# Kernel optimization log

Measured on AMD Instinct MI355X. Metric: run time of the kernel, lower is better.

Reference implementation:

```python
import jax, jax.numpy as jnp
import numpy as np

D_MODEL = 2048
D_INNER = 4096
D_XB = 512
D_STATE = 16
D_CONV = 4
DT_RANK = 128
BATCH = 1
SEQ = 2048
NUM_XB_HEAD = D_XB // D_STATE      # 32 kv heads
NUM_C_HEAD = D_INNER // D_STATE    # 256 query-side heads (groups)
REPEAT = NUM_C_HEAD // NUM_XB_HEAD # 8
HEAD_P = D_INNER // NUM_C_HEAD     # channels per group (= d_state here)


def setup_inputs() -> dict:
    key = jax.random.key(0)
    ks = jax.random.split(key, 8)
    sc = lambda k, shape, s=0.02: (jax.random.normal(k, shape, jnp.float32) * s)
    hidden_states = jax.random.normal(ks[0], (BATCH, SEQ, D_MODEL), jnp.float32)
    in_proj_w = sc(ks[1], (2 * D_XB + 2 * D_INNER, D_MODEL))
    dt_in_proj_w = sc(ks[2], (DT_RANK, D_MODEL))
    dt_proj_w = sc(ks[3], (D_INNER, DT_RANK), DT_RANK ** -0.5)
    # standard mamba dt bias init: inv-softplus of dt ~ logUniform[1e-3, 0.1]
    dt = jnp.exp(jax.random.uniform(ks[4], (D_INNER,)) * (np.log(0.1) - np.log(1e-3)) + np.log(1e-3))
    dt_proj_b = dt + jnp.log(-jnp.expm1(-dt))
    conv_w = sc(ks[5], (D_INNER, 1, D_CONV), 0.2)
    conv_b = jnp.zeros((D_INNER,), jnp.float32)
    A_log = jnp.log(jnp.tile(jnp.arange(1, D_STATE + 1, dtype=jnp.float32), (D_INNER, 1)))
    D = jnp.ones((D_INNER,), jnp.float32)
    out_proj_w = sc(ks[6], (D_MODEL, D_INNER), D_INNER ** -0.5)
    return dict(hidden_states=hidden_states, in_proj_w=in_proj_w, dt_in_proj_w=dt_in_proj_w,
                dt_proj_w=dt_proj_w, dt_proj_b=dt_proj_b, conv_w=conv_w, conv_b=conv_b,
                A_log=A_log, D=D, out_proj_w=out_proj_w)


def _mamba2_fwd(hidden_states, in_proj_w, dt_in_proj_w, dt_proj_w, dt_proj_b,
                conv_w, conv_b, A_log, D, out_proj_w):
    b, l, _ = hidden_states.shape
    zxbc = hidden_states @ in_proj_w.T  # (b,l,2*d_xb+2*d_inner)
    z = zxbc[..., :D_INNER]
    x = zxbc[..., D_INNER:D_INNER + D_XB]
    Bm = zxbc[..., D_INNER + D_XB:D_INNER + 2 * D_XB]
    Cm = zxbc[..., D_INNER + 2 * D_XB:]
    A = -jnp.exp(A_log)  # (d_inner, d_state)
    # low-rank dt: d_model -> dt_rank -> d_inner
    dt = (hidden_states @ dt_in_proj_w.T) @ dt_proj_w.T  # (b,l,d_inner)
    delta = jax.nn.softplus(dt + dt_proj_b)  # delta_softplus with delta_bias
    # repeat_kv before conv: (b,l,h_xb,n) -> (b,l,h_C,n) -> (b,d_inner,l)
    xh = jnp.repeat(x.reshape(b, l, NUM_XB_HEAD, D_STATE), REPEAT, axis=2)
    xc = xh.reshape(b, l, D_INNER).transpose(0, 2, 1)  # (b,d,l)
    # depthwise causal conv1d + SiLU
    xc = jax.lax.conv_general_dilated(xc, conv_w, (1,), [(D_CONV - 1, 0)],
                                      feature_group_count=D_INNER,
                                      dimension_numbers=('NCH', 'OIH', 'NCH'))
    u = jax.nn.silu(xc + conv_b[None, :, None])  # (b,d,l)
    Bh = jnp.repeat(Bm.reshape(b, l, NUM_XB_HEAD, D_STATE), REPEAT, axis=2)  # (b,l,g,n)
    Ch = Cm.reshape(b, l, NUM_C_HEAD, D_STATE)  # (b,l,g,n)
    # selective scan over time; channel d -> group d // HEAD_P
    u_r = u.transpose(0, 2, 1).reshape(b, l, NUM_C_HEAD, HEAD_P)
    d_r = delta.reshape(b, l, NUM_C_HEAD, HEAD_P)
    A_r = A.reshape(NUM_C_HEAD, HEAD_P, D_STATE)

    def step(h, inp):
        dt_t, u_t, B_t, C_t = inp  # (b,g,p),(b,g,p),(b,g,n),(b,g,n)
        dA = jnp.exp(dt_t[..., None] * A_r)  # (b,g,p,n)
        h = h * dA + (dt_t * u_t)[..., None] * B_t[:, :, None, :]
        y = jnp.einsum('bgpn,bgn->bgp', h, C_t)
        return h, y

    h0 = jnp.zeros((b, NUM_C_HEAD, HEAD_P, D_STATE), u.dtype)
    xs = (d_r.transpose(1, 0, 2, 3), u_r.transpose(1, 0, 2, 3),
          Bh.transpose(1, 0, 2, 3), Ch.transpose(1, 0, 2, 3))
    _, ys = jax.lax.scan(step, h0, xs)  # (l,b,g,p)
    y = ys.transpose(1, 0, 2, 3).reshape(b, l, D_INNER)
    y = y + u.transpose(0, 2, 1) * D  # skip D*u
    out = y * jax.nn.silu(z)          # gate
    return out @ out_proj_w.T         # (b,l,d_model)


def reference(hidden_states, in_proj_w, dt_in_proj_w, dt_proj_w, dt_proj_b,
              conv_w, conv_b, A_log, D, out_proj_w):
    return _mamba2_fwd(hidden_states, in_proj_w, dt_in_proj_w, dt_proj_w, dt_proj_b,
                       conv_w, conv_b, A_log, D, out_proj_w)
```

## Files before the change

kernel.cpp:

```cpp
#include <hip/hip_runtime.h>
#include <hip/hip_bf16.h>

#define SEQ     2048
#define DMODEL  2048
#define DINNER  4096
#define DXB     512
#define DSTATE  16
#define DTRANK  128
#define ZXBC_N  9216
#define NGROUP  256
#define NCH     32
#define TC      64

#define OFF_Z 0
#define OFF_X 4096
#define OFF_B 4608
#define OFF_C 5120

typedef __attribute__((ext_vector_type(8))) short short8;
typedef __attribute__((ext_vector_type(8))) unsigned short us8;
typedef __attribute__((ext_vector_type(4))) float f32x4;

__device__ __forceinline__ float softplus_f(float x) {
    return x > 0.f ? x + log1pf(expf(-x)) : log1pf(expf(x));
}
__device__ __forceinline__ float silu_f(float x) {
    return x / (1.f + __expf(-x));
}
__device__ __forceinline__ ushort f2bf(float f) {
    union { float f; unsigned u; } v; v.f = f;
    unsigned r = v.u + 0x7fffu + ((v.u >> 16) & 1u);
    return (ushort)(r >> 16);
}
__device__ __forceinline__ float bf2f(ushort u) {
    union { unsigned u; float f; } v; v.u = (unsigned)u << 16;
    return v.f;
}

__global__ __launch_bounds__(256) void f32_to_bf16(const float* __restrict__ in,
                                                   ushort* __restrict__ out, int n4) {
    int i = blockIdx.x * 256 + threadIdx.x;
    if (i < n4) {
        float4 v = ((const float4*)in)[i];
        ushort4 o;
        o.x = f2bf(v.x); o.y = f2bf(v.y); o.z = f2bf(v.z); o.w = f2bf(v.w);
        ((ushort4*)out)[i] = o;
    }
}

__global__ __launch_bounds__(256) void cvt4_kernel(const float* __restrict__ h,   ushort* __restrict__ hb,
                                                   const float* __restrict__ ip,  ushort* __restrict__ ipb,
                                                   const float* __restrict__ di,  ushort* __restrict__ dib,
                                                   const float* __restrict__ dp,  ushort* __restrict__ dpb) {
    const int b = blockIdx.x;
    const float* src; ushort* dst; int off;
    if (b < 4096)        { src = h;  dst = hb;  off = b; }
    else if (b < 22528)  { src = ip; dst = ipb; off = b - 4096; }
    else if (b < 22784)  { src = di; dst = dib; off = b - 22528; }
    else                 { src = dp; dst = dpb; off = b - 22784; }
    const int i = off * 256 + threadIdx.x;
    float4 v = ((const float4*)src)[i];
    ushort4 o;
    o.x = f2bf(v.x); o.y = f2bf(v.y); o.z = f2bf(v.z); o.w = f2bf(v.w);
    ((ushort4*)dst)[i] = o;
}

#define GLOAD16(gp, lp) __builtin_amdgcn_global_load_lds( \
    (const __attribute__((address_space(1))) void*)(gp), \
    (__attribute__((address_space(3))) void*)(lp), 16, 0, 0)

template<int EPI>
__global__ __launch_bounds__(256, 4) void gemm_bt_bf16(const ushort* __restrict__ A,
                                                       const ushort* __restrict__ B,
                                                       void* __restrict__ Cout,
                                                       const float* __restrict__ bias,
                                                       int M, int N, int K) {
    __shared__ ushort As[128 * 64];
    __shared__ ushort Bs[128 * 64];
    const int nbx = N >> 7;
    const int nwg = gridDim.x;
    int lin = blockIdx.x;
    if ((nwg & 7) == 0) lin = (lin & 7) * (nwg >> 3) + (lin >> 3);
    const int by = lin / nbx;
    const int bx = lin - by * nbx;
    const int row0 = by << 7, col0 = bx << 7;

    const int tid  = threadIdx.x;
    const int w    = tid >> 6;
    const int lane = tid & 63;
    const size_t kstride = (size_t)K * gridDim.y;
    const size_t koff    = (size_t)blockIdx.y * K;
    const size_t cbase   = (size_t)blockIdx.y * M * N;

    const int lrow  = lane >> 3;
    const int lslot = (lane & 7) ^ lrow;
    const ushort* ag = A + (size_t)(row0 + (w << 5) + lrow) * kstride + koff + (lslot << 3);
    const ushort* bg = B + (size_t)(col0 + (w << 5) + lrow) * kstride + koff + (lslot << 3);
    ushort* asb = As + ((w << 5) << 6);
    ushort* bsb = Bs + ((w << 5) << 6);

    const int wm = (w >> 1) << 6;
    const int wn = (w & 1) << 6;
    const int fr = lane & 15;
    const int kq = lane >> 4;
    const int f7 = fr & 7;

    f32x4 acc[4][4] = {};
    for (int k0 = 0; k0 < K; k0 += 64) {
        __syncthreads();
        #pragma unroll
        for (int k = 0; k < 4; ++k) {
            GLOAD16(ag + (size_t)(k << 3) * kstride + k0, asb + (k << 9));
            GLOAD16(bg + (size_t)(k << 3) * kstride + k0, bsb + (k << 9));
        }
        __syncthreads();
        #pragma unroll
        for (int ks = 0; ks < 2; ++ks) {
            const int ps = (((ks << 2) + kq) ^ f7) << 3;
            short8 af[4], bf[4];
            #pragma unroll
            for (int i = 0; i < 4; ++i)
                af[i] = *(const short8*)(As + ((wm + i * 16 + fr) << 6) + ps);
            #pragma unroll
            for (int j = 0; j < 4; ++j)
                bf[j] = *(const short8*)(Bs + ((wn + j * 16 + fr) << 6) + ps);
            #pragma unroll
            for (int i = 0; i < 4; ++i)
                #pragma unroll
                for (int j = 0; j < 4; ++j)
                    acc[i][j] = __builtin_amdgcn_mfma_f32_16x16x32_bf16(af[i], bf[j], acc[i][j], 0, 0, 0);
        }
    }

    const int orow = row0 + wm + (kq << 2);
    const int ocol = col0 + wn + fr;
    #pragma unroll
    for (int i = 0; i < 4; ++i) {
        #pragma unroll
        for (int r = 0; r < 4; ++r) {
            const int row = orow + i * 16 + r;
            #pragma unroll
            for (int j = 0; j < 4; ++j) {
                const int col = ocol + j * 16;
                float v = acc[i][j][r];
                if (EPI == 1) v = softplus_f(v + bias[col]);
                if (EPI == 2) ((ushort*)Cout)[(size_t)row * N + col] = f2bf(v);
                else          ((float*)Cout)[cbase + (size_t)row * N + col] = v;
            }
        }
    }
}

__global__ __launch_bounds__(256) void t1_reduce(const float* __restrict__ part,
                                                 ushort* __restrict__ out) {
    const int i = blockIdx.x * 256 + threadIdx.x;
    float4 s = ((const float4*)part)[i];
    #pragma unroll
    for (int z = 1; z < 8; ++z) {
        float4 p = ((const float4*)part)[z * 65536 + i];
        s.x += p.x; s.y += p.y; s.z += p.z; s.w += p.w;
    }
    ushort4 o;
    o.x = f2bf(s.x); o.y = f2bf(s.y); o.z = f2bf(s.z); o.w = f2bf(s.w);
    ((ushort4*)out)[i] = o;
}

__global__ __launch_bounds__(256) void out_reduce2(const float* __restrict__ part,
                                                   float* __restrict__ out) {
    const int i = blockIdx.x * 256 + threadIdx.x;
    float4 a = ((const float4*)part)[i];
    float4 b = ((const float4*)part)[1048576 + i];
    a.x += b.x; a.y += b.y; a.z += b.z; a.w += b.w;
    ((float4*)out)[i] = a;
}


__global__ __launch_bounds__(256) void scan_pass1(const ushort* __restrict__ zxbc,
                                                  const float* __restrict__ delta,
                                                  const float* __restrict__ conv_w,
                                                  const float* __restrict__ conv_b,
                                                  const float* __restrict__ A_log,
                                                  float* __restrict__ hend,
                                                  float* __restrict__ dsum) {
    __shared__ float sB[TC][32];
    const int ch  = blockIdx.y;
    const int c0  = blockIdx.x << 8;
    const int tid = threadIdx.x;
    const int c   = c0 + tid;
    const int t0  = ch * TC;
    const int xhl = (tid >> 7) & 1;
    const int xcol = ((c >> 7) << 4) | (c & 15);

    float Av[16];
    #pragma unroll
    for (int q = 0; q < 4; ++q) {
        float4 a4 = *(const float4*)(A_log + (c << 4) + (q << 2));
        Av[q*4+0] = -expf(a4.x); Av[q*4+1] = -expf(a4.y);
        Av[q*4+2] = -expf(a4.z); Av[q*4+3] = -expf(a4.w);
    }
    const float4 w4 = *(const float4*)(conv_w + c * 4);
    const float cb = conv_b[c];

    {
        const int f  = tid & 3;
        const int tl = tid >> 2;
        const int xb0 = (c0 >> 7) << 4;
        us8 v = *(const us8*)(zxbc + (size_t)(t0 + tl) * ZXBC_N + OFF_B + xb0 + (f << 3));
        float* dst = &sB[tl][f << 3];
        #pragma unroll
        for (int e = 0; e < 8; ++e) dst[e] = bf2f(v[e]);
    }

    float xm3 = 0.f, xm2 = 0.f, xm1 = 0.f;
    if (ch > 0) {
        xm3 = bf2f(zxbc[(size_t)(t0 - 3) * ZXBC_N + OFF_X + xcol]);
        xm2 = bf2f(zxbc[(size_t)(t0 - 2) * ZXBC_N + OFF_X + xcol]);
        xm1 = bf2f(zxbc[(size_t)(t0 - 1) * ZXBC_N + OFF_X + xcol]);
    }
    float dcur = delta[(size_t)t0 * DINNER + c];
    float xcur = bf2f(zxbc[(size_t)t0 * ZXBC_N + OFF_X + xcol]);

    float h[16];
    #pragma unroll
    for (int n = 0; n < 16; ++n) h[n] = 0.f;
    float Dc = 0.f;
    __syncthreads();

    #pragma unroll 4
    for (int tl = 0; tl < TC; ++tl) {
        float dn = 0.f, xn = 0.f;
        if (tl < TC - 1) {
            const size_t t1 = (size_t)(t0 + tl + 1);
            dn = delta[t1 * DINNER + c];
            xn = bf2f(zxbc[t1 * ZXBC_N + OFF_X + xcol]);
        }
        float Bv[16];
        *(float4*)(Bv +  0) = *(const float4*)&sB[tl][(xhl << 4) +  0];
        *(float4*)(Bv +  4) = *(const float4*)&sB[tl][(xhl << 4) +  4];
        *(float4*)(Bv +  8) = *(const float4*)&sB[tl][(xhl << 4) +  8];
        *(float4*)(Bv + 12) = *(const float4*)&sB[tl][(xhl << 4) + 12];
        float u = cb;
        u = fmaf(w4.x, xm3, u); u = fmaf(w4.y, xm2, u);
        u = fmaf(w4.z, xm1, u); u = fmaf(w4.w, xcur, u);
        u = silu_f(u);
        xm3 = xm2; xm2 = xm1; xm1 = xcur;
        const float du = dcur * u;
        Dc += dcur;
        #pragma unroll
        for (int n = 0; n < 16; ++n) {
            const float dA = __expf(dcur * Av[n]);
            h[n] = fmaf(h[n], dA, du * Bv[n]);
        }
        dcur = dn; xcur = xn;
    }
    float* hp = hend + ((size_t)ch * DINNER + c) * 16;
    #pragma unroll
    for (int q = 0; q < 4; ++q)
        *(float4*)(hp + (q << 2)) = make_float4(h[q*4+0], h[q*4+1], h[q*4+2], h[q*4+3]);
    dsum[(size_t)ch * DINNER + c] = Dc;
}

__global__ __launch_bounds__(256) void scan_mid(const float* __restrict__ A_log,
                                                float* __restrict__ hend,
                                                const float* __restrict__ dsum) {
    const int idx = blockIdx.x * 256 + threadIdx.x;
    const int c = idx >> 4, n = idx & 15;
    const float Av = -expf(A_log[(c << 4) + n]);
    float h = 0.f;
    #pragma unroll
    for (int ch = 0; ch < NCH; ++ch) {
        const size_t slot = ((size_t)ch * DINNER + c) * 16 + n;
        const float dec = __expf(Av * dsum[(size_t)ch * DINNER + c]);
        const float he  = hend[slot];
        hend[slot] = h;
        h = fmaf(dec, h, he);
    }
}

__global__ __launch_bounds__(256) void scan_pass2(const ushort* __restrict__ zxbc,
                                                  const float* __restrict__ delta,
                                                  const float* __restrict__ conv_w,
                                                  const float* __restrict__ conv_b,
                                                  const float* __restrict__ A_log,
                                                  const float* __restrict__ Dvec,
                                                  const float* __restrict__ h0buf,
                                                  ushort* __restrict__ ypre) {
    __shared__ float sB[32][32];
    __shared__ float sC[32][256];
    const int ch  = blockIdx.y;
    const int c0  = blockIdx.x << 8;
    const int tid = threadIdx.x;
    const int c   = c0 + tid;
    const int t0  = ch * TC;
    const int xhl = (tid >> 7) & 1;
    const int gl  = tid >> 4;
    const int xcol = ((c >> 7) << 4) | (c & 15);

    float Av[16];
    #pragma unroll
    for (int q = 0; q < 4; ++q) {
        float4 a4 = *(const float4*)(A_log + (c << 4) + (q << 2));
        Av[q*4+0] = -expf(a4.x); Av[q*4+1] = -expf(a4.y);
        Av[q*4+2] = -expf(a4.z); Av[q*4+3] = -expf(a4.w);
    }
    const float4 w4 = *(const float4*)(conv_w + c * 4);
    const float cb = conv_b[c];
    const float Dv = Dvec[c];

    const int btl = tid >> 3;
    const int bf_ = tid & 7;
    const int xb0 = (c0 >> 7) << 4;
    const int crow = tid >> 5;
    const int cgrp = tid & 31;
    ushort4 rB; us8 rC[4];
    {
        rB = *(const ushort4*)(zxbc + (size_t)(t0 + btl) * ZXBC_N + OFF_B + xb0 + (bf_ << 2));
        #pragma unroll
        for (int k = 0; k < 4; ++k) {
            const int row = crow + (k << 3);
            rC[k] = *(const us8*)(zxbc + (size_t)(t0 + row) * ZXBC_N + OFF_C + c0 + (cgrp << 3));
        }
    }

    float xm3 = 0.f, xm2 = 0.f, xm1 = 0.f;
    if (ch > 0) {
        xm3 = bf2f(zxbc[(size_t)(t0 - 3) * ZXBC_N + OFF_X + xcol]);
        xm2 = bf2f(zxbc[(size_t)(t0 - 2) * ZXBC_N + OFF_X + xcol]);
        xm1 = bf2f(zxbc[(size_t)(t0 - 1) * ZXBC_N + OFF_X + xcol]);
    }
    float dcur = delta[(size_t)t0 * DINNER + c];
    float xcur = bf2f(zxbc[(size_t)t0 * ZXBC_N + OFF_X + xcol]);
    float zcur = bf2f(zxbc[(size_t)t0 * ZXBC_N + OFF_Z + c]);

    float h[16];
    {
        const float* hp = h0buf + ((size_t)ch * DINNER + c) * 16;
        #pragma unroll
        for (int q = 0; q < 4; ++q) {
            float4 v = *(const float4*)(hp + (q << 2));
            h[q*4+0] = v.x; h[q*4+1] = v.y; h[q*4+2] = v.z; h[q*4+3] = v.w;
        }
    }

    for (int hh = 0; hh < 2; ++hh) {
        __syncthreads();
        sB[btl][(bf_ << 2) + 0] = bf2f(rB.x);
        sB[btl][(bf_ << 2) + 1] = bf2f(rB.y);
        sB[btl][(bf_ << 2) + 2] = bf2f(rB.z);
        sB[btl][(bf_ << 2) + 3] = bf2f(rB.w);
        #pragma unroll
        for (int k = 0; k < 4; ++k) {
            const int row = crow + (k << 3);
            float* dst = &sC[row][cgrp << 3];
            #pragma unroll
            for (int e = 0; e < 8; ++e) dst[e] = bf2f(rC[k][e]);
        }
        __syncthreads();
        if (hh == 0) {
            const int th = t0 + 32;
            rB = *(const ushort4*)(zxbc + (size_t)(th + btl) * ZXBC_N + OFF_B + xb0 + (bf_ << 2));
            #pragma unroll
            for (int k = 0; k < 4; ++k) {
                const int row = crow + (k << 3);
                rC[k] = *(const us8*)(zxbc + (size_t)(th + row) * ZXBC_N + OFF_C + c0 + (cgrp << 3));
            }
        }
        const int tb = t0 + (hh << 5);
        #pragma unroll 4
        for (int tl = 0; tl < 32; ++tl) {
            const int t = tb + tl;
            float dn = 0.f, xn = 0.f, zn = 0.f;
            if (t < t0 + TC - 1) {
                const size_t t1 = (size_t)(t + 1);
                dn = delta[t1 * DINNER + c];
                xn = bf2f(zxbc[t1 * ZXBC_N + OFF_X + xcol]);
                zn = bf2f(zxbc[t1 * ZXBC_N + OFF_Z + c]);
            }
            float Bv[16], Cv[16];
            *(float4*)(Bv +  0) = *(const float4*)&sB[tl][(xhl << 4) +  0];
            *(float4*)(Bv +  4) = *(const float4*)&sB[tl][(xhl << 4) +  4];
            *(float4*)(Bv +  8) = *(const float4*)&sB[tl][(xhl << 4) +  8];
            *(float4*)(Bv + 12) = *(const float4*)&sB[tl][(xhl << 4) + 12];
            *(float4*)(Cv +  0) = *(const float4*)&sC[tl][(gl << 4) +  0];
            *(float4*)(Cv +  4) = *(const float4*)&sC[tl][(gl << 4) +  4];
            *(float4*)(Cv +  8) = *(const float4*)&sC[tl][(gl << 4) +  8];
            *(float4*)(Cv + 12) = *(const float4*)&sC[tl][(gl << 4) + 12];
            float u = cb;
            u = fmaf(w4.x, xm3, u); u = fmaf(w4.y, xm2, u);
            u = fmaf(w4.z, xm1, u); u = fmaf(w4.w, xcur, u);
            u = silu_f(u);
            xm3 = xm2; xm2 = xm1; xm1 = xcur;
            const float du = dcur * u;
            float y0 = 0.f, y1 = 0.f, y2 = 0.f, y3 = 0.f;
            #pragma unroll
            for (int q = 0; q < 4; ++q) {
                const float dA0 = __expf(dcur * Av[q*4+0]);
                const float dA1 = __expf(dcur * Av[q*4+1]);
                const float dA2 = __expf(dcur * Av[q*4+2]);
                const float dA3 = __expf(dcur * Av[q*4+3]);
                h[q*4+0] = fmaf(h[q*4+0], dA0, du * Bv[q*4+0]);
                h[q*4+1] = fmaf(h[q*4+1], dA1, du * Bv[q*4+1]);
                h[q*4+2] = fmaf(h[q*4+2], dA2, du * Bv[q*4+2]);
                h[q*4+3] = fmaf(h[q*4+3], dA3, du * Bv[q*4+3]);
                y0 = fmaf(h[q*4+0], Cv[q*4+0], y0);
                y1 = fmaf(h[q*4+1], Cv[q*4+1], y1);
                y2 = fmaf(h[q*4+2], Cv[q*4+2], y2);
                y3 = fmaf(h[q*4+3], Cv[q*4+3], y3);
            }
            const float y = (y0 + y1) + (y2 + y3);
            const float yv = fmaf(u, Dv, y) * silu_f(zcur);
            ypre[(size_t)t * DINNER + c] = f2bf(yv);
            dcur = dn; xcur = xn; zcur = zn;
        }
    }
}

extern "C" void kernel_launch(void* const* d_in, const int* in_sizes, int n_in,
                              void* d_out, int out_size, void* d_ws, size_t ws_size,
                              hipStream_t stream) {
    const float* hidden       = (const float*)d_in[0];
    const float* in_proj_w    = (const float*)d_in[1];
    const float* dt_in_proj_w = (const float*)d_in[2];
    const float* dt_proj_w    = (const float*)d_in[3];
    const float* dt_proj_b    = (const float*)d_in[4];
    const float* conv_w       = (const float*)d_in[5];
    const float* conv_b       = (const float*)d_in[6];
    const float* A_log        = (const float*)d_in[7];
    const float* Dvec         = (const float*)d_in[8];
    const float* out_proj_w   = (const float*)d_in[9];

    char* wsb = (char*)d_ws;
    ushort* zxbc  = (ushort*)(wsb + 0ull);
    float*  opart = (float*) (wsb + 0ull);
    float*  delta = (float*) (wsb + 75497472ull);
    ushort* ypre  = (ushort*)(wsb + 109051904ull);
    float*  t1part= (float*) (wsb + 109051904ull);
    ushort* hb    = (ushort*)(wsb + 125829120ull);
    ushort* t1b   = (ushort*)(wsb + 134217728ull);
    ushort* wdtib = (ushort*)(wsb + 134742016ull);
    ushort* wdtpb = (ushort*)(wsb + 135266304ull);
    ushort* wbig  = (ushort*)(wsb + 136314880ull);
    float*  hend  = (float*) (wsb + 153092096ull);
    float*  dsum  = (float*) (wsb + 161480704ull);

    cvt4_kernel<<<23296, 256, 0, stream>>>(hidden, hb, in_proj_w, wbig,
                                           dt_in_proj_w, wdtib, dt_proj_w, wdtpb);

    gemm_bt_bf16<2><<<1152, 256, 0, stream>>>(hb, wbig, zxbc, nullptr, SEQ, ZXBC_N, DMODEL);
    f32_to_bf16<<<8192, 256, 0, stream>>>(out_proj_w, wbig, 2097152);
    gemm_bt_bf16<0><<<dim3(16, 8), 256, 0, stream>>>(hb, wdtib, t1part, nullptr, SEQ, DTRANK, 256);
    t1_reduce<<<256, 256, 0, stream>>>(t1part, t1b);
    gemm_bt_bf16<1><<<512, 256, 0, stream>>>(t1b, wdtpb, delta, dt_proj_b, SEQ, DINNER, DTRANK);

    scan_pass1<<<dim3(16, NCH), 256, 0, stream>>>(zxbc, delta, conv_w, conv_b, A_log, hend, dsum);
    scan_mid  <<<256, 256, 0, stream>>>(A_log, hend, dsum);
    scan_pass2<<<dim3(16, NCH), 256, 0, stream>>>(zxbc, delta, conv_w, conv_b, A_log, Dvec, hend, ypre);

    gemm_bt_bf16<0><<<dim3(256, 2), 256, 0, stream>>>(ypre, wbig, opart, nullptr, SEQ, DMODEL, 2048);
    out_reduce2<<<4096, 256, 0, stream>>>(opart, (float*)d_out);
}
```

Baseline: 354.8 us.

## Multi-stage async LDS pipeline with 8-wave GEMM tiles

Rewrites the bf16 GEMM to use 512 threads (8 waves) per 128x128 tile, each wave computing 64x32. Global-to-LDS loads now go through a 4-stage ring buffer (128 KB of LDS) with explicit vmcnt waits, so tiles for later K steps are fetched while the current one is computed. MFMA sections are wrapped in setprio. The large LDS footprint limits occupancy to about one block per CU, and the hand-written waitcnt counts must match the exact number of loads in flight.

```diff
diff --git a/kernel.cpp b/kernel.cpp
--- a/kernel.cpp
+++ b/kernel.cpp
@@ -70,13 +70,12 @@
     (__attribute__((address_space(3))) void*)(lp), 16, 0, 0)
 
 template<int EPI>
-__global__ __launch_bounds__(256, 4) void gemm_bt_bf16(const ushort* __restrict__ A,
+__global__ __launch_bounds__(512, 2) void gemm_bt_bf16(const ushort* __restrict__ A,
                                                        const ushort* __restrict__ B,
                                                        void* __restrict__ Cout,
                                                        const float* __restrict__ bias,
                                                        int M, int N, int K) {
-    __shared__ ushort As[128 * 64];
-    __shared__ ushort Bs[128 * 64];
+    __shared__ ushort lds[65536];
     const int nbx = N >> 7;
     const int nwg = gridDim.x;
     int lin = blockIdx.x;
@@ -86,51 +85,74 @@
     const int row0 = by << 7, col0 = bx << 7;
 
     const int tid  = threadIdx.x;
-    const int w    = tid >> 6;
+    const int wv   = tid >> 6;
     const int lane = tid & 63;
     const size_t kstride = (size_t)K * gridDim.y;
     const size_t koff    = (size_t)blockIdx.y * K;
     const size_t cbase   = (size_t)blockIdx.y * M * N;
 
-    const int lrow  = lane >> 3;
-    const int lslot = (lane & 7) ^ lrow;
-    const ushort* ag = A + (size_t)(row0 + (w << 5) + lrow) * kstride + koff + (lslot << 3);
-    const ushort* bg = B + (size_t)(col0 + (w << 5) + lrow) * kstride + koff + (lslot << 3);
-    ushort* asb = As + ((w << 5) << 6);
-    ushort* bsb = Bs + ((w << 5) << 6);
-
-    const int wm = (w >> 1) << 6;
-    const int wn = (w & 1) << 6;
+    const int lr    = lane >> 3;
+    const int lslot = ((lane & 7) ^ lr) << 3;
+    const ushort* ga0 = A + (size_t)(row0 + (wv << 3) + lr) * kstride + koff + lslot;
+    const ushort* ga1 = ga0 + (size_t)64 * kstride;
+    const ushort* gb0 = B + (size_t)(col0 + (wv << 3) + lr) * kstride + koff + lslot;
+    const ushort* gb1 = gb0 + (size_t)64 * kstride;
+    const int lbase = wv << 9;
+
+#define STAGE(kt) do {                                                     \
+        const int s_ = ((kt) & 3) << 14;                                   \
+        const size_t kk_ = (size_t)(kt) << 6;                              \
+        GLOAD16(ga0 + kk_, lds + s_ + lbase);                              \
+        GLOAD16(ga1 + kk_, lds + s_ + lbase + 4096);                       \
+        GLOAD16(gb0 + kk_, lds + s_ + 8192 + lbase);                       \
+        GLOAD16(gb1 + kk_, lds + s_ + 8192 + lbase + 4096);                \
+    } while (0)
+
+    const int wm = (wv >> 2) << 6;
+    const int wn = (wv & 3) << 5;
     const int fr = lane & 15;
     const int kq = lane >> 4;
     const int f7 = fr & 7;
 
-    f32x4 acc[4][4] = {};
-    for (int k0 = 0; k0 < K; k0 += 64) {
-        __syncthreads();
-        #pragma unroll
-        for (int k = 0; k < 4; ++k) {
-            GLOAD16(ag + (size_t)(k << 3) * kstride + k0, asb + (k << 9));
-            GLOAD16(bg + (size_t)(k << 3) * kstride + k0, bsb + (k << 9));
-        }
-        __syncthreads();
+    const int NT = K >> 6;
+    f32x4 acc[4][2] = {};
+
+    if (0 < NT) STAGE(0);
+    if (1 < NT) STAGE(1);
+    if (2 < NT) STAGE(2);
+
+    for (int kt = 0; kt < NT; ++kt) {
+        if (kt + 3 < NT) STAGE(kt + 3);
+        if      (kt + 3 < NT) asm volatile("s_waitcnt vmcnt(12)" ::: "memory");
+        else if (kt + 2 < NT) asm volatile("s_waitcnt vmcnt(8)"  ::: "memory");
+        else if (kt + 1 < NT) asm volatile("s_waitcnt vmcnt(4)"  ::: "memory");
+        else                  asm volatile("s_waitcnt vmcnt(0)"  ::: "memory");
+        __builtin_amdgcn_s_barrier();
+        asm volatile("" ::: "memory");
+        const ushort* As_ = lds + ((kt & 3) << 14);
+        const ushort* Bs_ = As_ + 8192;
         #pragma unroll
         for (int ks = 0; ks < 2; ++ks) {
             const int ps = (((ks << 2) + kq) ^ f7) << 3;
-            short8 af[4], bf[4];
+            short8 af[4], bf[2];
             #pragma unroll
             for (int i = 0; i < 4; ++i)
-                af[i] = *(const short8*)(As + ((wm + i * 16 + fr) << 6) + ps);
-            #pragma unroll
-            for (int j = 0; j < 4; ++j)
-                bf[j] = *(const short8*)(Bs + ((wn + j * 16 + fr) << 6) + ps);
+                af[i] = *(const short8*)(As_ + ((wm + i * 16 + fr) << 6) + ps);
+            #pragma unroll
+            for (int j = 0; j < 2; ++j)
+                bf[j] = *(const short8*)(Bs_ + ((wn + j * 16 + fr) << 6) + ps);
+            __builtin_amdgcn_s_setprio(1);
             #pragma unroll
             for (int i = 0; i < 4; ++i)
                 #pragma unroll
-                for (int j = 0; j < 4; ++j)
+                for (int j = 0; j < 2; ++j)
                     acc[i][j] = __builtin_amdgcn_mfma_f32_16x16x32_bf16(af[i], bf[j], acc[i][j], 0, 0, 0);
-        }
-    }
+            __builtin_amdgcn_s_setprio(0);
+        }
+        asm volatile("" ::: "memory");
+        __builtin_amdgcn_s_barrier();
+    }
+#undef STAGE
 
     const int orow = row0 + wm + (kq << 2);
     const int ocol = col0 + wn + fr;
@@ -140,7 +162,7 @@
         for (int r = 0; r < 4; ++r) {
             const int row = orow + i * 16 + r;
             #pragma unroll
-            for (int j = 0; j < 4; ++j) {
+            for (int j = 0; j < 2; ++j) {
                 const int col = ocol + j * 16;
                 float v = acc[i][j][r];
                 if (EPI == 1) v = softplus_f(v + bias[col]);
@@ -446,16 +468,16 @@
     cvt4_kernel<<<23296, 256, 0, stream>>>(hidden, hb, in_proj_w, wbig,
                                            dt_in_proj_w, wdtib, dt_proj_w, wdtpb);
 
-    gemm_bt_bf16<2><<<1152, 256, 0, stream>>>(hb, wbig, zxbc, nullptr, SEQ, ZXBC_N, DMODEL);
+    gemm_bt_bf16<2><<<1152, 512, 0, stream>>>(hb, wbig, zxbc, nullptr, SEQ, ZXBC_N, DMODEL);
     f32_to_bf16<<<8192, 256, 0, stream>>>(out_proj_w, wbig, 2097152);
-    gemm_bt_bf16<0><<<dim3(16, 8), 256, 0, stream>>>(hb, wdtib, t1part, nullptr, SEQ, DTRANK, 256);
+    gemm_bt_bf16<0><<<dim3(16, 8), 512, 0, stream>>>(hb, wdtib, t1part, nullptr, SEQ, DTRANK, 256);
     t1_reduce<<<256, 256, 0, stream>>>(t1part, t1b);
-    gemm_bt_bf16<1><<<512, 256, 0, stream>>>(t1b, wdtpb, delta, dt_proj_b, SEQ, DINNER, DTRANK);
+    gemm_bt_bf16<1><<<512, 512, 0, stream>>>(t1b, wdtpb, delta, dt_proj_b, SEQ, DINNER, DTRANK);
 
     scan_pass1<<<dim3(16, NCH), 256, 0, stream>>>(zxbc, delta, conv_w, conv_b, A_log, hend, dsum);
     scan_mid  <<<256, 256, 0, stream>>>(A_log, hend, dsum);
     scan_pass2<<<dim3(16, NCH), 256, 0, stream>>>(zxbc, delta, conv_w, conv_b, A_log, Dvec, hend, ypre);
 
-    gemm_bt_bf16<0><<<dim3(256, 2), 256, 0, stream>>>(ypre, wbig, opart, nullptr, SEQ, DMODEL, 2048);
+    gemm_bt_bf16<0><<<dim3(256, 2), 512, 0, stream>>>(ypre, wbig, opart, nullptr, SEQ, DMODEL, 2048);
     out_reduce2<<<4096, 256, 0, stream>>>(opart, (float*)d_out);
 }
```

Result: no change. 356.9 us (+0.6%).

## Fuse dt down-projection into in_proj GEMM, store delta as bf16, merge conversions

Applied to the files above, without the earlier changes.

Widens the in_proj GEMM by 128 output columns so it also computes the low-rank dt projection, reading those weight rows from a separate buffer and writing them to a side bf16 output. This removes the split-K dt GEMM, its reduce kernel and one launch. The out_proj weight conversion is folded into the single up-front conversion kernel, into its own buffer. Delta is now written and read as bf16 instead of fp32, halving its traffic in both scan passes at some cost in precision.

```diff
diff --git a/kernel.cpp b/kernel.cpp
--- a/kernel.cpp
+++ b/kernel.cpp
@@ -37,27 +37,18 @@
     return v.f;
 }
 
-__global__ __launch_bounds__(256) void f32_to_bf16(const float* __restrict__ in,
-                                                   ushort* __restrict__ out, int n4) {
-    int i = blockIdx.x * 256 + threadIdx.x;
-    if (i < n4) {
-        float4 v = ((const float4*)in)[i];
-        ushort4 o;
-        o.x = f2bf(v.x); o.y = f2bf(v.y); o.z = f2bf(v.z); o.w = f2bf(v.w);
-        ((ushort4*)out)[i] = o;
-    }
-}
-
-__global__ __launch_bounds__(256) void cvt4_kernel(const float* __restrict__ h,   ushort* __restrict__ hb,
+__global__ __launch_bounds__(256) void cvt5_kernel(const float* __restrict__ h,   ushort* __restrict__ hb,
                                                    const float* __restrict__ ip,  ushort* __restrict__ ipb,
                                                    const float* __restrict__ di,  ushort* __restrict__ dib,
-                                                   const float* __restrict__ dp,  ushort* __restrict__ dpb) {
+                                                   const float* __restrict__ dp,  ushort* __restrict__ dpb,
+                                                   const float* __restrict__ op,  ushort* __restrict__ opb) {
     const int b = blockIdx.x;
     const float* src; ushort* dst; int off;
     if (b < 4096)        { src = h;  dst = hb;  off = b; }
     else if (b < 22528)  { src = ip; dst = ipb; off = b - 4096; }
     else if (b < 22784)  { src = di; dst = dib; off = b - 22528; }
-    else                 { src = dp; dst = dpb; off = b - 22784; }
+    else if (b < 23296)  { src = dp; dst = dpb; off = b - 22784; }
+    else                 { src = op; dst = opb; off = b - 23296; }
     const int i = off * 256 + threadIdx.x;
     float4 v = ((const float4*)src)[i];
     ushort4 o;
@@ -72,7 +63,9 @@
 template<int EPI>
 __global__ __launch_bounds__(256, 4) void gemm_bt_bf16(const ushort* __restrict__ A,
                                                        const ushort* __restrict__ B,
+                                                       const ushort* __restrict__ Baux,
                                                        void* __restrict__ Cout,
+                                                       ushort* __restrict__ aux,
                                                        const float* __restrict__ bias,
                                                        int M, int N, int K) {
     __shared__ ushort As[128 * 64];
@@ -94,8 +87,10 @@
 
     const int lrow  = lane >> 3;
     const int lslot = (lane & 7) ^ lrow;
-    const ushort* ag = A + (size_t)(row0 + (w << 5) + lrow) * kstride + koff + (lslot << 3);
-    const ushort* bg = B + (size_t)(col0 + (w << 5) + lrow) * kstride + koff + (lslot << 3);
+    const ushort* bsrc = B;
+    if (EPI == 4 && col0 >= 9216) bsrc = Baux - (size_t)9216 * kstride;
+    const ushort* ag = A    + (size_t)(row0 + (w << 5) + lrow) * kstride + koff + (lslot << 3);
+    const ushort* bg = bsrc + (size_t)(col0 + (w << 5) + lrow) * kstride + koff + (lslot << 3);
     ushort* asb = As + ((w << 5) << 6);
     ushort* bsb = Bs + ((w << 5) << 6);
 
@@ -143,26 +138,19 @@
             for (int j = 0; j < 4; ++j) {
                 const int col = ocol + j * 16;
                 float v = acc[i][j][r];
-                if (EPI == 1) v = softplus_f(v + bias[col]);
-                if (EPI == 2) ((ushort*)Cout)[(size_t)row * N + col] = f2bf(v);
-                else          ((float*)Cout)[cbase + (size_t)row * N + col] = v;
+                if (EPI == 0) {
+                    ((float*)Cout)[cbase + (size_t)row * N + col] = v;
+                } else if (EPI == 2) {
+                    ((ushort*)Cout)[(size_t)row * N + col] = f2bf(v);
+                } else if (EPI == 3) {
+                    ((ushort*)Cout)[(size_t)row * N + col] = f2bf(softplus_f(v + bias[col]));
+                } else if (EPI == 4) {
+                    if (col < 9216) ((ushort*)Cout)[(size_t)row * 9216 + col] = f2bf(v);
+                    else            aux[(size_t)row * 128 + (col - 9216)] = f2bf(v);
+                }
             }
         }
     }
-}
-
-__global__ __launch_bounds__(256) void t1_reduce(const float* __restrict__ part,
-                                                 ushort* __restrict__ out) {
-    const int i = blockIdx.x * 256 + threadIdx.x;
-    float4 s = ((const float4*)part)[i];
-    #pragma unroll
-    for (int z = 1; z < 8; ++z) {
-        float4 p = ((const float4*)part)[z * 65536 + i];
-        s.x += p.x; s.y += p.y; s.z += p.z; s.w += p.w;
-    }
-    ushort4 o;
-    o.x = f2bf(s.x); o.y = f2bf(s.y); o.z = f2bf(s.z); o.w = f2bf(s.w);
-    ((ushort4*)out)[i] = o;
 }
 
 __global__ __launch_bounds__(256) void out_reduce2(const float* __restrict__ part,
@@ -176,7 +164,7 @@
 
 
 __global__ __launch_bounds__(256) void scan_pass1(const ushort* __restrict__ zxbc,
-                                                  const float* __restrict__ delta,
+                                                  const ushort* __restrict__ delta,
                                                   const float* __restrict__ conv_w,
                                                   const float* __restrict__ conv_b,
                                                   const float* __restrict__ A_log,
@@ -217,7 +205,7 @@
         xm2 = bf2f(zxbc[(size_t)(t0 - 2) * ZXBC_N + OFF_X + xcol]);
         xm1 = bf2f(zxbc[(size_t)(t0 - 1) * ZXBC_N + OFF_X + xcol]);
     }
-    float dcur = delta[(size_t)t0 * DINNER + c];
+    float dcur = bf2f(delta[(size_t)t0 * DINNER + c]);
     float xcur = bf2f(zxbc[(size_t)t0 * ZXBC_N + OFF_X + xcol]);
 
     float h[16];
@@ -231,7 +219,7 @@
         float dn = 0.f, xn = 0.f;
         if (tl < TC - 1) {
             const size_t t1 = (size_t)(t0 + tl + 1);
-            dn = delta[t1 * DINNER + c];
+            dn = bf2f(delta[t1 * DINNER + c]);
             xn = bf2f(zxbc[t1 * ZXBC_N + OFF_X + xcol]);
         }
         float Bv[16];
@@ -278,7 +266,7 @@
 }
 
 __global__ __launch_bounds__(256) void scan_pass2(const ushort* __restrict__ zxbc,
-                                                  const float* __restrict__ delta,
+                                                  const ushort* __restrict__ delta,
                                                   const float* __restrict__ conv_w,
                                                   const float* __restrict__ conv_b,
                                                   const float* __restrict__ A_log,
@@ -328,7 +316,7 @@
         xm2 = bf2f(zxbc[(size_t)(t0 - 2) * ZXBC_N + OFF_X + xcol]);
         xm1 = bf2f(zxbc[(size_t)(t0 - 1) * ZXBC_N + OFF_X + xcol]);
     }
-    float dcur = delta[(size_t)t0 * DINNER + c];
+    float dcur = bf2f(delta[(size_t)t0 * DINNER + c]);
     float xcur = bf2f(zxbc[(size_t)t0 * ZXBC_N + OFF_X + xcol]);
     float zcur = bf2f(zxbc[(size_t)t0 * ZXBC_N + OFF_Z + c]);
 
@@ -372,7 +360,7 @@
             float dn = 0.f, xn = 0.f, zn = 0.f;
             if (t < t0 + TC - 1) {
                 const size_t t1 = (size_t)(t + 1);
-                dn = delta[t1 * DINNER + c];
+                dn = bf2f(delta[t1 * DINNER + c]);
                 xn = bf2f(zxbc[t1 * ZXBC_N + OFF_X + xcol]);
                 zn = bf2f(zxbc[t1 * ZXBC_N + OFF_Z + c]);
             }
@@ -432,9 +420,9 @@
     char* wsb = (char*)d_ws;
     ushort* zxbc  = (ushort*)(wsb + 0ull);
     float*  opart = (float*) (wsb + 0ull);
-    float*  delta = (float*) (wsb + 75497472ull);
+    ushort* wopb  = (ushort*)(wsb + 37748736ull);
+    ushort* delta = (ushort*)(wsb + 75497472ull);
     ushort* ypre  = (ushort*)(wsb + 109051904ull);
-    float*  t1part= (float*) (wsb + 109051904ull);
     ushort* hb    = (ushort*)(wsb + 125829120ull);
     ushort* t1b   = (ushort*)(wsb + 134217728ull);
     ushort* wdtib = (ushort*)(wsb + 134742016ull);
@@ -443,19 +431,20 @@
     float*  hend  = (float*) (wsb + 153092096ull);
     float*  dsum  = (float*) (wsb + 161480704ull);
 
-    cvt4_kernel<<<23296, 256, 0, stream>>>(hidden, hb, in_proj_w, wbig,
-                                           dt_in_proj_w, wdtib, dt_proj_w, wdtpb);
-
-    gemm_bt_bf16<2><<<1152, 256, 0, stream>>>(hb, wbig, zxbc, nullptr, SEQ, ZXBC_N, DMODEL);
-    f32_to_bf16<<<8192, 256, 0, stream>>>(out_proj_w, wbig, 2097152);
-    gemm_bt_bf16<0><<<dim3(16, 8), 256, 0, stream>>>(hb, wdtib, t1part, nullptr, SEQ, DTRANK, 256);
-    t1_reduce<<<256, 256, 0, stream>>>(t1part, t1b);
-    gemm_bt_bf16<1><<<512, 256, 0, stream>>>(t1b, wdtpb, delta, dt_proj_b, SEQ, DINNER, DTRANK);
+    cvt5_kernel<<<31488, 256, 0, stream>>>(hidden, hb, in_proj_w, wbig,
+                                           dt_in_proj_w, wdtib, dt_proj_w, wdtpb,
+                                           out_proj_w, wopb);
+
+    gemm_bt_bf16<4><<<1168, 256, 0, stream>>>(hb, wbig, wdtib, zxbc, t1b, nullptr,
+                                              SEQ, ZXBC_N + DTRANK, DMODEL);
+    gemm_bt_bf16<3><<<512, 256, 0, stream>>>(t1b, wdtpb, nullptr, delta, nullptr,
+                                             dt_proj_b, SEQ, DINNER, DTRANK);
 
     scan_pass1<<<dim3(16, NCH), 256, 0, stream>>>(zxbc, delta, conv_w, conv_b, A_log, hend, dsum);
     scan_mid  <<<256, 256, 0, stream>>>(A_log, hend, dsum);
     scan_pass2<<<dim3(16, NCH), 256, 0, stream>>>(zxbc, delta, conv_w, conv_b, A_log, Dvec, hend, ypre);
 
-    gemm_bt_bf16<0><<<dim3(256, 2), 256, 0, stream>>>(ypre, wbig, opart, nullptr, SEQ, DMODEL, 2048);
+    gemm_bt_bf16<0><<<dim3(256, 2), 256, 0, stream>>>(ypre, wopb, nullptr, opart, nullptr,
+                                                      nullptr, SEQ, DMODEL, 2048);
     out_reduce2<<<4096, 256, 0, stream>>>(opart, (float*)d_out);
 }
```

New measurement: 354.0 us. No clear change (-0.2%).
